# Performance work log

Hardware: AMD Instinct MI355X
Metric: run time of the kernel (lower is better)

Reference implementation:

```python
import jax, jax.numpy as jnp
import numpy as np

N_USERS = 100000
N_ITEMS = 50000
N_NODES = N_USERS + N_ITEMS
LATENT = 64
NNZ = 2400000
BATCH = 2048
EPS = 1e-12  # F.normalize eps


def setup_inputs() -> dict:
    key = jax.random.key(0)
    ks = jax.random.split(key, 16)
    inp = {
        "rows": jax.random.randint(ks[0], (NNZ,), 0, N_NODES, dtype=jnp.int32),
        "cols": jax.random.randint(ks[1], (NNZ,), 0, N_NODES, dtype=jnp.int32),
        "vals": jax.random.uniform(ks[2], (NNZ,), dtype=jnp.float32),
        "x": jax.random.normal(ks[3], (N_NODES, LATENT), dtype=jnp.float32) * 0.1,
        "users": jax.random.randint(ks[12], (BATCH,), 0, N_USERS, dtype=jnp.int32),
        "items": jax.random.randint(ks[13], (BATCH,), 0, N_ITEMS, dtype=jnp.int32),
    }
    for k in range(2):
        inp[f"W_gc{k}"] = jax.random.normal(ks[4 + 4 * k], (LATENT, LATENT), dtype=jnp.float32) * 0.1
        inp[f"b_gc{k}"] = jax.random.normal(ks[5 + 4 * k], (1, LATENT), dtype=jnp.float32) * 0.1
        inp[f"W_bi{k}"] = jax.random.normal(ks[6 + 4 * k], (LATENT, LATENT), dtype=jnp.float32) * 0.1
        inp[f"b_bi{k}"] = jax.random.normal(ks[7 + 4 * k], (1, LATENT), dtype=jnp.float32) * 0.1
    return inp


def _l2_normalize(v):
    # F.normalize(p=2, dim=1): divide by max(||v||_2, eps)
    n = jnp.sqrt(jnp.sum(v * v, axis=1, keepdims=True))
    return v / jnp.maximum(n, EPS)


def reference(rows, cols, vals, x,
              W_gc0, b_gc0, W_bi0, b_bi0,
              W_gc1, b_gc1, W_bi1, b_bi1,
              users, items):
    weights = [(W_gc0, b_gc0, W_bi0, b_bi0), (W_gc1, b_gc1, W_bi1, b_bi1)]
    ego = x                      # [N, D]
    embs = [x]
    for (Wg, bg, Wb, bb) in weights:
        # sparse adj @ ego  (COO gather + segment-sum scatter)
        msgs = vals[:, None] * ego[cols]                              # [nnz, D]
        side = jax.ops.segment_sum(msgs, rows, num_segments=N_NODES)  # [N, D]
        sum_emb = side @ Wg + bg
        bi_emb = (ego * side) @ Wb + bb
        ego = _l2_normalize(jax.nn.leaky_relu(sum_emb + bi_emb, negative_slope=0.2))
        embs.append(ego)
    all_emb = jnp.concatenate(embs, axis=1)          # [N, 3*D]
    users_emb = all_emb[users]                       # [B, 3*D]
    items_emb = all_emb[N_USERS + items]             # [B, 3*D]
    gamma = jnp.sum(users_emb * items_emb, axis=1)   # [B]
    return gamma
```

## Files before the change

### kernel.cpp

```cpp
#include <hip/hip_runtime.h>

#define N_USERS_C 100000
#define N_NODES_C 150000
#define D 64
#define NB 2344
#define NSUP 74
#define CPAD 16
#define TILE1 32
#define SPAD 33
#define SPAD2 17
#define FCAP 1536
#define S1B 256
#define FRAG 240
#define S2CAP 2560
#define BPS 16
#define FPB (S1B / BPS)
#define NSCAN 147
#define MARK 1

__global__ __launch_bounds__(256) void mark1_k(
    const int* __restrict__ u, const int* __restrict__ it,
    unsigned char* __restrict__ samp, unsigned char* __restrict__ need, int batch)
{
    int i = blockIdx.x * blockDim.x + threadIdx.x;
    if (i >= 2 * batch) return;
    int n = (i < batch) ? u[i] : N_USERS_C + it[i - batch];
    samp[n] = MARK;
    need[n] = MARK;
}

__global__ __launch_bounds__(256) void mark2_k(
    const int* __restrict__ rows, const int* __restrict__ cols,
    const unsigned char* __restrict__ samp, unsigned char* __restrict__ need, int nnz)
{
    int gtid = blockIdx.x * blockDim.x + threadIdx.x;
    int stride = gridDim.x * blockDim.x;
    for (int e = gtid; e < nnz; e += stride)
        if (samp[rows[e]] == MARK) need[cols[e]] = MARK;
}

__global__ __launch_bounds__(1024) void scan1_k(
    const unsigned char* __restrict__ need, int* __restrict__ part,
    int* __restrict__ bsum, int n)
{
    __shared__ int wsum[16];
    int i = blockIdx.x * 1024 + threadIdx.x;
    int lane = threadIdx.x & 63, wid = threadIdx.x >> 6;
    int v = (i < n && need[i] == MARK) ? 1 : 0;
    int incl = v;
    #pragma unroll
    for (int off = 1; off < 64; off <<= 1) {
        int t = __shfl_up(incl, off);
        if (lane >= off) incl += t;
    }
    if (lane == 63) wsum[wid] = incl;
    __syncthreads();
    int woff = 0;
    for (int w = 0; w < wid; ++w) woff += wsum[w];
    if (i < n) part[i] = woff + incl - v;
    if (threadIdx.x == 1023) bsum[blockIdx.x] = woff + incl;
}

__global__ __launch_bounds__(256) void scanB_k(
    const int* __restrict__ bsum, int* __restrict__ idx,
    const unsigned char* __restrict__ need, int* __restrict__ list,
    int* __restrict__ bcur, int* __restrict__ Mptr, int n)
{
    __shared__ int pre[NSCAN + 1];
    __shared__ int raw[NSCAN];
    int t = threadIdx.x;
    if (t < NSCAN) raw[t] = bsum[t];
    __syncthreads();
    if (t == 0) {
        int run = 0;
        for (int k = 0; k < NSCAN; ++k) { pre[k] = run; run += raw[k]; }
        pre[NSCAN] = run;
    }
    __syncthreads();
    int i = blockIdx.x * blockDim.x + t;
    if (i < NB) bcur[i * CPAD] = i * FCAP;
    if (blockIdx.x == 0 && t == 0) Mptr[0] = pre[NSCAN];
    if (i >= n) return;
    int val = idx[i] + pre[i >> 10];
    if (need[i] == MARK) { idx[i] = val; list[val] = i; }
    else idx[i] = -1;
}

__global__ __launch_bounds__(512) void s1_k(
    const int* __restrict__ rows, const int* __restrict__ cols,
    const float* __restrict__ vals, const int* __restrict__ idx,
    int2* __restrict__ pairs1, int* __restrict__ scnt, int nnz)
{
    __shared__ int lcur[NSUP];
    int t = threadIdx.x;
    for (int i = t; i < NSUP; i += 512) lcur[i] = 0;
    __syncthreads();
    int b = blockIdx.x;
    int per = (nnz + S1B - 1) / S1B;
    int s = b * per;
    int e = min(nnz, s + per);
    for (int i = s + t; i < e; i += 512) {
        int ci = idx[rows[i]];
        if (ci < 0) continue;
        int sp = ci >> 11;
        int k = atomicAdd(&lcur[sp], 1);
        pairs1[(size_t)sp * (S1B * FRAG) + b * FRAG + k] =
            make_int2(((ci & 2047) << 18) | cols[i], __float_as_int(vals[i]));
    }
    __syncthreads();
    for (int i = t; i < NSUP; i += 512) scnt[i * S1B + b] = lcur[i];
}

__global__ __launch_bounds__(256) void s2_k(
    const int* __restrict__ scnt, const int2* __restrict__ pairs1,
    int* __restrict__ bcurP, int2* __restrict__ pairs)
{
    __shared__ int2 sbuf[S2CAP];
    __shared__ int fcnt[32], fcur[32], gb[32];
    int sp = blockIdx.x / BPS, part = blockIdx.x % BPS;
    int t = threadIdx.x;
    if (t < 32) { fcnt[t] = 0; fcur[t] = 0; }
    __syncthreads();
    int base = 0;
    for (int fi = 0; fi < FPB; ++fi) {
        int b = part * FPB + fi;
        int m = scnt[sp * S1B + b];
        const int2* src = &pairs1[(size_t)sp * (S1B * FRAG) + b * FRAG];
        for (int i = t; i < m; i += 256) {
            int2 p = src[i];
            sbuf[base + i] = p;
            atomicAdd(&fcnt[(p.x >> 18) >> 6], 1);
        }
        base += m;
    }
    __syncthreads();
    if (t < 32) {
        int c = fcnt[t];
        gb[t] = c ? atomicAdd(&bcurP[(sp * 32 + t) * CPAD], c) : 0;
    }
    __syncthreads();
    for (int i = t; i < base; i += 256) {
        int2 p = sbuf[i];
        int ris = p.x >> 18;
        int f = ris >> 6;
        int k = atomicAdd(&fcur[f], 1);
        pairs[gb[f] + k] = make_int2(((ris & 63) << 18) | (p.x & 0x3FFFF), p.y);
    }
}

__global__ __launch_bounds__(256) void sortb_k(
    const int* __restrict__ bcurP, int2* __restrict__ pairs,
    int* __restrict__ rp)
{
    __shared__ int2 buf[FCAP];
    __shared__ int cnt[64];
    __shared__ int cur[64];
    int b = blockIdx.x;
    int s = b * FCAP;
    int e = bcurP[b * CPAD];
    int m = e - s;
    int t = threadIdx.x;
    if (t < 64) cnt[t] = 0;
    __syncthreads();
    for (int i = t; i < m; i += 256) {
        int2 p = pairs[s + i];
        buf[i] = p;
        atomicAdd(&cnt[p.x >> 18], 1);
    }
    __syncthreads();
    if (t < 64) {
        int v = cnt[t];
        int incl = v;
        #pragma unroll
        for (int o = 1; o < 64; o <<= 1) {
            int u = __shfl_up(incl, o);
            if (t >= o) incl += u;
        }
        cur[t] = incl - v;
        rp[b * 65 + t] = s + incl - v;
        if (t == 63) rp[b * 65 + 64] = s + incl;
    }
    __syncthreads();
    for (int i = t; i < m; i += 256) {
        int2 p = buf[i];
        int dst = atomicAdd(&cur[p.x >> 18], 1);
        pairs[s + dst] = make_int2(p.x & 0x3FFFF, p.y);
    }
}

__global__ __launch_bounds__(128, 4) void fuse1_k(
    const int* __restrict__ rp, const int2* __restrict__ pairs,
    const float* __restrict__ x,
    const float* __restrict__ Wg, const float* __restrict__ bg,
    const float* __restrict__ Wb, const float* __restrict__ bb,
    float* __restrict__ out, const int* __restrict__ list,
    const int* __restrict__ Mptr)
{
    __shared__ __align__(16) float sAT[D][SPAD];
    __shared__ __align__(16) float sBT[D][SPAD];

    int nr = Mptr[0];
    int r0 = blockIdx.x * TILE1;
    if (r0 >= nr) return;

    int t    = threadIdx.x;
    int lane = t & 63;
    int wid  = t >> 6;
    int lq   = lane & 15;
    int qb   = lane & 48;

    for (int pass = 0; pass < 4; ++pass) {
        int rr  = wid * 16 + pass * 4 + (lane >> 4);
        int row = r0 + rr;
        int valid = row < nr;
        int s = 0, len = 0, er = 0;
        if (valid) {
            int rb = (row >> 6) * 65 + (row & 63);
            s = rp[rb];
            len = rp[rb + 1] - s;
            er = list[row];
        }
        int ml = len;
        ml = max(ml, __shfl_xor(ml, 16));
        ml = max(ml, __shfl_xor(ml, 32));

        float4 acc = make_float4(0.f, 0.f, 0.f, 0.f);
        for (int base = 0; base < ml; base += 16) {
            int2 p = make_int2(0, 0);
            int o = base + lq;
            if (o < len) p = pairs[s + o];
            int rem = len - base;
            rem = min(max(rem, 0), 16);
            int mr = rem;
            mr = max(mr, __shfl_xor(mr, 16));
            mr = max(mr, __shfl_xor(mr, 32));
            int cnt8 = (mr + 7) & ~7;
            for (int j = 0; j < cnt8; j += 8) {
                int c[8]; float v[8]; float4 f[8];
                #pragma unroll
                for (int q = 0; q < 8; ++q) {
                    c[q] = __shfl(p.x, qb | (j + q));
                    v[q] = __int_as_float(__shfl(p.y, qb | (j + q)));
                }
                #pragma unroll
                for (int q = 0; q < 8; ++q)
                    f[q] = *(const float4*)&x[(size_t)c[q] * D + lq * 4];
                #pragma unroll
                for (int q = 0; q < 8; ++q) {
                    acc.x = fmaf(v[q], f[q].x, acc.x);
                    acc.y = fmaf(v[q], f[q].y, acc.y);
                    acc.z = fmaf(v[q], f[q].z, acc.z);
                    acc.w = fmaf(v[q], f[q].w, acc.w);
                }
            }
        }
        float4 ev = make_float4(0.f, 0.f, 0.f, 0.f);
        if (valid) ev = *(const float4*)&x[(size_t)er * D + lq * 4];
        sAT[lq * 4 + 0][rr] = acc.x;
        sAT[lq * 4 + 1][rr] = acc.y;
        sAT[lq * 4 + 2][rr] = acc.z;
        sAT[lq * 4 + 3][rr] = acc.w;
        sBT[lq * 4 + 0][rr] = acc.x * ev.x;
        sBT[lq * 4 + 1][rr] = acc.y * ev.y;
        sBT[lq * 4 + 2][rr] = acc.z * ev.z;
        sBT[lq * 4 + 3][rr] = acc.w * ev.w;
    }
    __syncthreads();

    int tc = t & 15;
    int tr = t >> 4;
    float acc2[4][4] = {};
    #pragma unroll 4
    for (int k = 0; k < D; ++k) {
        float av[4] = {sAT[k][tr], sAT[k][tr + 8], sAT[k][tr + 16], sAT[k][tr + 24]};
        float bv[4] = {sBT[k][tr], sBT[k][tr + 8], sBT[k][tr + 16], sBT[k][tr + 24]};
        float4 g4 = *(const float4*)&Wg[k * D + tc * 4];
        float4 w4 = *(const float4*)&Wb[k * D + tc * 4];
        float gv[4] = {g4.x, g4.y, g4.z, g4.w};
        float wv[4] = {w4.x, w4.y, w4.z, w4.w};
        #pragma unroll
        for (int i = 0; i < 4; ++i)
            #pragma unroll
            for (int j = 0; j < 4; ++j)
                acc2[i][j] = fmaf(av[i], gv[j], fmaf(bv[i], wv[j], acc2[i][j]));
    }

    float4 bgv = *(const float4*)&bg[tc * 4];
    float4 bbv = *(const float4*)&bb[tc * 4];
    float bias[4] = {bgv.x + bbv.x, bgv.y + bbv.y, bgv.z + bbv.z, bgv.w + bbv.w};

    float vv[4][4];
    float ss[4] = {0.f, 0.f, 0.f, 0.f};
    #pragma unroll
    for (int i = 0; i < 4; ++i) {
        #pragma unroll
        for (int j = 0; j < 4; ++j) {
            float v = acc2[i][j] + bias[j];
            v = (v > 0.0f) ? v : 0.2f * v;
            vv[i][j] = v;
            ss[i] += v * v;
        }
    }
    #pragma unroll
    for (int i = 0; i < 4; ++i) {
        #pragma unroll
        for (int off = 1; off < 16; off <<= 1)
            ss[i] += __shfl_xor(ss[i], off);
    }
    #pragma unroll
    for (int i = 0; i < 4; ++i) {
        int row = r0 + tr + i * 8;
        if (row < nr) {
            int er2 = list[row];
            float inv = 1.0f / fmaxf(sqrtf(ss[i]), 1e-12f);
            float4 o = make_float4(vv[i][0] * inv, vv[i][1] * inv,
                                   vv[i][2] * inv, vv[i][3] * inv);
            *(float4*)&out[(size_t)er2 * D + tc * 4] = o;
        }
    }
}

__global__ __launch_bounds__(256, 4) void fuse2_k(
    const int* __restrict__ rp, const int2* __restrict__ pairs,
    const float* __restrict__ e1, const int* __restrict__ idx,
    const float* __restrict__ Wg, const float* __restrict__ bg,
    const float* __restrict__ Wb, const float* __restrict__ bb,
    float* __restrict__ out, const int* __restrict__ u,
    const int* __restrict__ it, int batch)
{
    __shared__ __align__(16) float sAT[D][SPAD2];
    __shared__ __align__(16) float sBT[D][SPAD2];

    int nr = 2 * batch;
    int r0 = blockIdx.x * 16;
    if (r0 >= nr) return;

    int t    = threadIdx.x;
    int lane = t & 63;
    int wid  = t >> 6;
    int lq   = lane & 15;
    int qb   = lane & 48;

    {
        int rr  = wid * 4 + (lane >> 4);
        int row = r0 + rr;
        int valid = row < nr;
        int s = 0, len = 0, n = 0;
        if (valid) {
            n = (row < batch) ? u[row] : N_USERS_C + it[row - batch];
            int cr = idx[n];
            int rb = (cr >> 6) * 65 + (cr & 63);
            s = rp[rb];
            len = rp[rb + 1] - s;
        }
        int ml = len;
        ml = max(ml, __shfl_xor(ml, 16));
        ml = max(ml, __shfl_xor(ml, 32));

        float4 acc = make_float4(0.f, 0.f, 0.f, 0.f);
        for (int base = 0; base < ml; base += 16) {
            int2 p = make_int2(0, 0);
            int o = base + lq;
            if (o < len) p = pairs[s + o];
            int rem = len - base;
            rem = min(max(rem, 0), 16);
            int mr = rem;
            mr = max(mr, __shfl_xor(mr, 16));
            mr = max(mr, __shfl_xor(mr, 32));
            int cnt8 = (mr + 7) & ~7;
            for (int j = 0; j < cnt8; j += 8) {
                int c[8]; float v[8]; float4 f[8];
                #pragma unroll
                for (int q = 0; q < 8; ++q) {
                    c[q] = __shfl(p.x, qb | (j + q));
                    v[q] = __int_as_float(__shfl(p.y, qb | (j + q)));
                }
                #pragma unroll
                for (int q = 0; q < 8; ++q)
                    f[q] = *(const float4*)&e1[(size_t)c[q] * D + lq * 4];
                #pragma unroll
                for (int q = 0; q < 8; ++q) {
                    acc.x = fmaf(v[q], f[q].x, acc.x);
                    acc.y = fmaf(v[q], f[q].y, acc.y);
                    acc.z = fmaf(v[q], f[q].z, acc.z);
                    acc.w = fmaf(v[q], f[q].w, acc.w);
                }
            }
        }
        float4 ev = make_float4(0.f, 0.f, 0.f, 0.f);
        if (valid) ev = *(const float4*)&e1[(size_t)n * D + lq * 4];
        sAT[lq * 4 + 0][rr] = acc.x;
        sAT[lq * 4 + 1][rr] = acc.y;
        sAT[lq * 4 + 2][rr] = acc.z;
        sAT[lq * 4 + 3][rr] = acc.w;
        sBT[lq * 4 + 0][rr] = acc.x * ev.x;
        sBT[lq * 4 + 1][rr] = acc.y * ev.y;
        sBT[lq * 4 + 2][rr] = acc.z * ev.z;
        sBT[lq * 4 + 3][rr] = acc.w * ev.w;
    }
    __syncthreads();

    int tc = t & 15;
    int tr = t >> 4;
    float acc2[4] = {};
    #pragma unroll 4
    for (int k = 0; k < D; ++k) {
        float a0 = sAT[k][tr];
        float b0 = sBT[k][tr];
        float4 g4 = *(const float4*)&Wg[k * D + tc * 4];
        float4 w4 = *(const float4*)&Wb[k * D + tc * 4];
        float gv[4] = {g4.x, g4.y, g4.z, g4.w};
        float wv[4] = {w4.x, w4.y, w4.z, w4.w};
        #pragma unroll
        for (int j = 0; j < 4; ++j)
            acc2[j] = fmaf(a0, gv[j], fmaf(b0, wv[j], acc2[j]));
    }

    float4 bgv = *(const float4*)&bg[tc * 4];
    float4 bbv = *(const float4*)&bb[tc * 4];
    float bias[4] = {bgv.x + bbv.x, bgv.y + bbv.y, bgv.z + bbv.z, bgv.w + bbv.w};

    float vv[4];
    float ss = 0.f;
    #pragma unroll
    for (int j = 0; j < 4; ++j) {
        float v = acc2[j] + bias[j];
        v = (v > 0.0f) ? v : 0.2f * v;
        vv[j] = v;
        ss += v * v;
    }
    #pragma unroll
    for (int off = 1; off < 16; off <<= 1)
        ss += __shfl_xor(ss, off);

    int row = r0 + tr;
    if (row < nr) {
        float inv = 1.0f / fmaxf(sqrtf(ss), 1e-12f);
        float4 o = make_float4(vv[0] * inv, vv[1] * inv, vv[2] * inv, vv[3] * inv);
        *(float4*)&out[(size_t)row * D + tc * 4] = o;
    }
}

__global__ __launch_bounds__(256) void gamma_k(
    const float* __restrict__ x, const float* __restrict__ e1,
    const float* __restrict__ e2c,
    const int* __restrict__ users, const int* __restrict__ items,
    float* __restrict__ gamma, int batch)
{
    int gtid = blockIdx.x * blockDim.x + threadIdx.x;
    int wave = gtid >> 6;
    int lane = threadIdx.x & 63;
    if (wave >= batch) return;
    size_t uu = (size_t)users[wave];
    size_t tt = (size_t)(N_USERS_C + items[wave]);
    float acc = x[uu * D + lane] * x[tt * D + lane]
              + e1[uu * D + lane] * e1[tt * D + lane]
              + e2c[(size_t)wave * D + lane] * e2c[(size_t)(batch + wave) * D + lane];
    #pragma unroll
    for (int off = 1; off < 64; off <<= 1) acc += __shfl_xor(acc, off);
    if (lane == 0) gamma[wave] = acc;
}

extern "C" void kernel_launch(void* const* d_in, const int* in_sizes, int n_in,
                              void* d_out, int out_size, void* d_ws, size_t ws_size,
                              hipStream_t stream) {
    const int*   rows  = (const int*)d_in[0];
    const int*   cols  = (const int*)d_in[1];
    const float* vals  = (const float*)d_in[2];
    const float* x     = (const float*)d_in[3];
    const int*   users = (const int*)d_in[4];
    const int*   items = (const int*)d_in[5];
    const float* Wg0 = (const float*)d_in[6];
    const float* bg0 = (const float*)d_in[7];
    const float* Wb0 = (const float*)d_in[8];
    const float* bb0 = (const float*)d_in[9];
    const float* Wg1 = (const float*)d_in[10];
    const float* bg1 = (const float*)d_in[11];
    const float* Wb1 = (const float*)d_in[12];
    const float* bb1 = (const float*)d_in[13];

    int nnz   = in_sizes[0];
    int batch = in_sizes[4];
    float* out = (float*)d_out;

    size_t emb = (size_t)N_NODES_C * D;
    float* A      = (float*)d_ws;
    float* Sbuf   = A + emb;
    int*   bcur   = (int*)(Sbuf + emb);
    int*   rp     = bcur + NB * CPAD;
    int*   idx    = rp + NB * 65 + 2;
    int*   list   = idx + N_NODES_C;
    int*   bsum   = list + N_NODES_C;
    int*   Mptr   = bsum + 1024;
    int*   scnt   = Mptr + 4;
    unsigned char* need = (unsigned char*)(scnt + NSUP * S1B);
    unsigned char* samp = need + N_NODES_C;
    int2*  pairs  = (int2*)(((size_t)(samp + N_NODES_C) + 15) & ~(size_t)15);

    int2*  pairs1 = (int2*)Sbuf;
    float* e2c    = Sbuf;

    mark1_k<<<(2 * batch + 255) / 256, 256, 0, stream>>>(users, items, samp, need, batch);
    mark2_k<<<1024, 256, 0, stream>>>(rows, cols, samp, need, nnz);
    scan1_k<<<NSCAN, 1024, 0, stream>>>(need, idx, bsum, N_NODES_C);
    scanB_k<<<(N_NODES_C + 255) / 256, 256, 0, stream>>>(bsum, idx, need, list, bcur, Mptr, N_NODES_C);

    s1_k<<<S1B, 512, 0, stream>>>(rows, cols, vals, idx, pairs1, scnt, nnz);
    s2_k<<<NSUP * BPS, 256, 0, stream>>>(scnt, pairs1, bcur, pairs);
    sortb_k<<<NB, 256, 0, stream>>>(bcur, pairs, rp);

    fuse1_k<<<(N_NODES_C + TILE1 - 1) / TILE1, 128, 0, stream>>>(
        rp, pairs, x, Wg0, bg0, Wb0, bb0, A, list, Mptr);

    fuse2_k<<<(2 * batch + 15) / 16, 256, 0, stream>>>(
        rp, pairs, A, idx, Wg1, bg1, Wb1, bb1, e2c, users, items, batch);

    gamma_k<<<(batch * 64 + 255) / 256, 256, 0, stream>>>(
        x, A, e2c, users, items, out, batch);
}
```

Baseline: 243.6 us.

## Replace three-pass bucket sort with degree-histogram CSR build and atomic scatter

The three-stage bucketed sort (s1/s2/sortb) that grouped edges by compacted row is replaced. Row degrees are now counted with global atomics inside the mark pass, prefix-scanned alongside the need flags, and edges of needed rows are scattered straight into a full-node CSR using per-row atomic cursors. This drops two kernel launches and the intermediate pairs1 staging traffic. In exchange it adds 2.4M global atomics for the degree count, plus scatter atomics, and the writes to pairs become random.

```diff
diff --git a/kernel.cpp b/kernel.cpp
--- a/kernel.cpp
+++ b/kernel.cpp
@@ -3,194 +3,114 @@
 #define N_USERS_C 100000
 #define N_NODES_C 150000
 #define D 64
-#define NB 2344
-#define NSUP 74
-#define CPAD 16
 #define TILE1 32
 #define SPAD 33
 #define SPAD2 17
-#define FCAP 1536
-#define S1B 256
-#define FRAG 240
-#define S2CAP 2560
-#define BPS 16
-#define FPB (S1B / BPS)
 #define NSCAN 147
 #define MARK 1
 
-__global__ __launch_bounds__(256) void mark1_k(
+__global__ __launch_bounds__(256) void mark1z_k(
     const int* __restrict__ u, const int* __restrict__ it,
-    unsigned char* __restrict__ samp, unsigned char* __restrict__ need, int batch)
+    unsigned char* __restrict__ samp, unsigned char* __restrict__ need,
+    int* __restrict__ dega, int batch, int n)
 {
     int i = blockIdx.x * blockDim.x + threadIdx.x;
-    if (i >= 2 * batch) return;
-    int n = (i < batch) ? u[i] : N_USERS_C + it[i - batch];
-    samp[n] = MARK;
-    need[n] = MARK;
-}
-
-__global__ __launch_bounds__(256) void mark2_k(
+    if (i < n) dega[i] = 0;
+    if (i < 2 * batch) {
+        int nd = (i < batch) ? u[i] : N_USERS_C + it[i - batch];
+        samp[nd] = MARK;
+        need[nd] = MARK;
+    }
+}
+
+__global__ __launch_bounds__(256) void mark2h_k(
     const int* __restrict__ rows, const int* __restrict__ cols,
-    const unsigned char* __restrict__ samp, unsigned char* __restrict__ need, int nnz)
+    const unsigned char* __restrict__ samp, unsigned char* __restrict__ need,
+    int* __restrict__ dega, int nnz)
 {
     int gtid = blockIdx.x * blockDim.x + threadIdx.x;
     int stride = gridDim.x * blockDim.x;
-    for (int e = gtid; e < nnz; e += stride)
-        if (samp[rows[e]] == MARK) need[cols[e]] = MARK;
-}
-
-__global__ __launch_bounds__(1024) void scan1_k(
-    const unsigned char* __restrict__ need, int* __restrict__ part,
-    int* __restrict__ bsum, int n)
-{
-    __shared__ int wsum[16];
+    for (int e = gtid; e < nnz; e += stride) {
+        int r = rows[e];
+        atomicAdd(&dega[r], 1);
+        if (samp[r] == MARK) need[cols[e]] = MARK;
+    }
+}
+
+__global__ __launch_bounds__(1024) void scan1x_k(
+    const unsigned char* __restrict__ need, const int* __restrict__ dega,
+    int* __restrict__ part, int* __restrict__ partd,
+    int* __restrict__ bsum, int* __restrict__ bsumd, int n)
+{
+    __shared__ int wsum[16], wsumd[16];
     int i = blockIdx.x * 1024 + threadIdx.x;
     int lane = threadIdx.x & 63, wid = threadIdx.x >> 6;
-    int v = (i < n && need[i] == MARK) ? 1 : 0;
-    int incl = v;
+    int f = (i < n && need[i] == MARK) ? 1 : 0;
+    int d = (i < n) ? dega[i] : 0;
+    int fi = f, di = d;
     #pragma unroll
     for (int off = 1; off < 64; off <<= 1) {
-        int t = __shfl_up(incl, off);
-        if (lane >= off) incl += t;
-    }
-    if (lane == 63) wsum[wid] = incl;
+        int t1 = __shfl_up(fi, off);
+        int t2 = __shfl_up(di, off);
+        if (lane >= off) { fi += t1; di += t2; }
+    }
+    if (lane == 63) { wsum[wid] = fi; wsumd[wid] = di; }
     __syncthreads();
-    int woff = 0;
-    for (int w = 0; w < wid; ++w) woff += wsum[w];
-    if (i < n) part[i] = woff + incl - v;
-    if (threadIdx.x == 1023) bsum[blockIdx.x] = woff + incl;
-}
-
-__global__ __launch_bounds__(256) void scanB_k(
-    const int* __restrict__ bsum, int* __restrict__ idx,
+    int wo = 0, wod = 0;
+    for (int w = 0; w < wid; ++w) { wo += wsum[w]; wod += wsumd[w]; }
+    if (i < n) { part[i] = wo + fi - f; partd[i] = wod + di - d; }
+    if (threadIdx.x == 1023) { bsum[blockIdx.x] = wo + fi; bsumd[blockIdx.x] = wod + di; }
+}
+
+__global__ __launch_bounds__(256) void scanBx_k(
+    const int* __restrict__ bsum, const int* __restrict__ bsumd,
+    const int* __restrict__ part, const int* __restrict__ partd,
     const unsigned char* __restrict__ need, int* __restrict__ list,
-    int* __restrict__ bcur, int* __restrict__ Mptr, int n)
+    int* __restrict__ rps, int* __restrict__ cur,
+    int* __restrict__ Mptr, int n)
 {
     __shared__ int pre[NSCAN + 1];
-    __shared__ int raw[NSCAN];
+    __shared__ int prd[NSCAN + 1];
+    __shared__ int raw[NSCAN], rawd[NSCAN];
     int t = threadIdx.x;
-    if (t < NSCAN) raw[t] = bsum[t];
+    if (t < NSCAN) { raw[t] = bsum[t]; rawd[t] = bsumd[t]; }
     __syncthreads();
     if (t == 0) {
-        int run = 0;
-        for (int k = 0; k < NSCAN; ++k) { pre[k] = run; run += raw[k]; }
-        pre[NSCAN] = run;
+        int rf = 0, rd = 0;
+        for (int k = 0; k < NSCAN; ++k) {
+            pre[k] = rf; rf += raw[k];
+            prd[k] = rd; rd += rawd[k];
+        }
+        pre[NSCAN] = rf; prd[NSCAN] = rd;
     }
     __syncthreads();
     int i = blockIdx.x * blockDim.x + t;
-    if (i < NB) bcur[i * CPAD] = i * FCAP;
     if (blockIdx.x == 0 && t == 0) Mptr[0] = pre[NSCAN];
     if (i >= n) return;
-    int val = idx[i] + pre[i >> 10];
-    if (need[i] == MARK) { idx[i] = val; list[val] = i; }
-    else idx[i] = -1;
-}
-
-__global__ __launch_bounds__(512) void s1_k(
+    int P = partd[i] + prd[i >> 10];
+    rps[i] = P;
+    cur[i] = P;
+    if (need[i] == MARK) list[part[i] + pre[i >> 10]] = i;
+}
+
+__global__ __launch_bounds__(256) void scatter_k(
     const int* __restrict__ rows, const int* __restrict__ cols,
-    const float* __restrict__ vals, const int* __restrict__ idx,
-    int2* __restrict__ pairs1, int* __restrict__ scnt, int nnz)
-{
-    __shared__ int lcur[NSUP];
-    int t = threadIdx.x;
-    for (int i = t; i < NSUP; i += 512) lcur[i] = 0;
-    __syncthreads();
-    int b = blockIdx.x;
-    int per = (nnz + S1B - 1) / S1B;
-    int s = b * per;
-    int e = min(nnz, s + per);
-    for (int i = s + t; i < e; i += 512) {
-        int ci = idx[rows[i]];
-        if (ci < 0) continue;
-        int sp = ci >> 11;
-        int k = atomicAdd(&lcur[sp], 1);
-        pairs1[(size_t)sp * (S1B * FRAG) + b * FRAG + k] =
-            make_int2(((ci & 2047) << 18) | cols[i], __float_as_int(vals[i]));
-    }
-    __syncthreads();
-    for (int i = t; i < NSUP; i += 512) scnt[i * S1B + b] = lcur[i];
-}
-
-__global__ __launch_bounds__(256) void s2_k(
-    const int* __restrict__ scnt, const int2* __restrict__ pairs1,
-    int* __restrict__ bcurP, int2* __restrict__ pairs)
-{
-    __shared__ int2 sbuf[S2CAP];
-    __shared__ int fcnt[32], fcur[32], gb[32];
-    int sp = blockIdx.x / BPS, part = blockIdx.x % BPS;
-    int t = threadIdx.x;
-    if (t < 32) { fcnt[t] = 0; fcur[t] = 0; }
-    __syncthreads();
-    int base = 0;
-    for (int fi = 0; fi < FPB; ++fi) {
-        int b = part * FPB + fi;
-        int m = scnt[sp * S1B + b];
-        const int2* src = &pairs1[(size_t)sp * (S1B * FRAG) + b * FRAG];
-        for (int i = t; i < m; i += 256) {
-            int2 p = src[i];
-            sbuf[base + i] = p;
-            atomicAdd(&fcnt[(p.x >> 18) >> 6], 1);
-        }
-        base += m;
-    }
-    __syncthreads();
-    if (t < 32) {
-        int c = fcnt[t];
-        gb[t] = c ? atomicAdd(&bcurP[(sp * 32 + t) * CPAD], c) : 0;
-    }
-    __syncthreads();
-    for (int i = t; i < base; i += 256) {
-        int2 p = sbuf[i];
-        int ris = p.x >> 18;
-        int f = ris >> 6;
-        int k = atomicAdd(&fcur[f], 1);
-        pairs[gb[f] + k] = make_int2(((ris & 63) << 18) | (p.x & 0x3FFFF), p.y);
-    }
-}
-
-__global__ __launch_bounds__(256) void sortb_k(
-    const int* __restrict__ bcurP, int2* __restrict__ pairs,
-    int* __restrict__ rp)
-{
-    __shared__ int2 buf[FCAP];
-    __shared__ int cnt[64];
-    __shared__ int cur[64];
-    int b = blockIdx.x;
-    int s = b * FCAP;
-    int e = bcurP[b * CPAD];
-    int m = e - s;
-    int t = threadIdx.x;
-    if (t < 64) cnt[t] = 0;
-    __syncthreads();
-    for (int i = t; i < m; i += 256) {
-        int2 p = pairs[s + i];
-        buf[i] = p;
-        atomicAdd(&cnt[p.x >> 18], 1);
-    }
-    __syncthreads();
-    if (t < 64) {
-        int v = cnt[t];
-        int incl = v;
-        #pragma unroll
-        for (int o = 1; o < 64; o <<= 1) {
-            int u = __shfl_up(incl, o);
-            if (t >= o) incl += u;
-        }
-        cur[t] = incl - v;
-        rp[b * 65 + t] = s + incl - v;
-        if (t == 63) rp[b * 65 + 64] = s + incl;
-    }
-    __syncthreads();
-    for (int i = t; i < m; i += 256) {
-        int2 p = buf[i];
-        int dst = atomicAdd(&cur[p.x >> 18], 1);
-        pairs[s + dst] = make_int2(p.x & 0x3FFFF, p.y);
+    const float* __restrict__ vals, const unsigned char* __restrict__ need,
+    int* __restrict__ cur, int2* __restrict__ pairs, int nnz)
+{
+    int gtid = blockIdx.x * blockDim.x + threadIdx.x;
+    int stride = gridDim.x * blockDim.x;
+    for (int e = gtid; e < nnz; e += stride) {
+        int r = rows[e];
+        if (need[r] != MARK) continue;
+        int pos = atomicAdd(&cur[r], 1);
+        pairs[pos] = make_int2(cols[e], __float_as_int(vals[e]));
     }
 }
 
 __global__ __launch_bounds__(128, 4) void fuse1_k(
-    const int* __restrict__ rp, const int2* __restrict__ pairs,
-    const float* __restrict__ x,
+    const int* __restrict__ rps, const int* __restrict__ curp,
+    const int2* __restrict__ pairs, const float* __restrict__ x,
     const float* __restrict__ Wg, const float* __restrict__ bg,
     const float* __restrict__ Wb, const float* __restrict__ bb,
     float* __restrict__ out, const int* __restrict__ list,
@@ -215,10 +135,9 @@
         int valid = row < nr;
         int s = 0, len = 0, er = 0;
         if (valid) {
-            int rb = (row >> 6) * 65 + (row & 63);
-            s = rp[rb];
-            len = rp[rb + 1] - s;
             er = list[row];
+            s = rps[er];
+            len = curp[er] - s;
         }
         int ml = len;
         ml = max(ml, __shfl_xor(ml, 16));
@@ -321,8 +240,8 @@
 }
 
 __global__ __launch_bounds__(256, 4) void fuse2_k(
-    const int* __restrict__ rp, const int2* __restrict__ pairs,
-    const float* __restrict__ e1, const int* __restrict__ idx,
+    const int* __restrict__ rps, const int* __restrict__ curp,
+    const int2* __restrict__ pairs, const float* __restrict__ e1,
     const float* __restrict__ Wg, const float* __restrict__ bg,
     const float* __restrict__ Wb, const float* __restrict__ bb,
     float* __restrict__ out, const int* __restrict__ u,
@@ -348,10 +267,8 @@
         int s = 0, len = 0, n = 0;
         if (valid) {
             n = (row < batch) ? u[row] : N_USERS_C + it[row - batch];
-            int cr = idx[n];
-            int rb = (cr >> 6) * 65 + (cr & 63);
-            s = rp[rb];
-            len = rp[rb + 1] - s;
+            s = rps[n];
+            len = curp[n] - s;
         }
         int ml = len;
         ml = max(ml, __shfl_xor(ml, 16));
@@ -486,34 +403,36 @@
     size_t emb = (size_t)N_NODES_C * D;
     float* A      = (float*)d_ws;
     float* Sbuf   = A + emb;
-    int*   bcur   = (int*)(Sbuf + emb);
-    int*   rp     = bcur + NB * CPAD;
-    int*   idx    = rp + NB * 65 + 2;
-    int*   list   = idx + N_NODES_C;
-    int*   bsum   = list + N_NODES_C;
-    int*   Mptr   = bsum + 1024;
-    int*   scnt   = Mptr + 4;
-    unsigned char* need = (unsigned char*)(scnt + NSUP * S1B);
+    int*   rps    = (int*)(Sbuf + emb);
+    int*   cur    = rps + N_NODES_C;
+    int*   dega   = cur + N_NODES_C;
+    int*   list   = dega + N_NODES_C;
+    int*   part   = list + N_NODES_C;
+    int*   partd  = part + N_NODES_C;
+    int*   bsum   = partd + N_NODES_C;
+    int*   bsumd  = bsum + 1024;
+    int*   Mptr   = bsumd + 1024;
+    unsigned char* need = (unsigned char*)(Mptr + 4);
     unsigned char* samp = need + N_NODES_C;
     int2*  pairs  = (int2*)(((size_t)(samp + N_NODES_C) + 15) & ~(size_t)15);
 
-    int2*  pairs1 = (int2*)Sbuf;
     float* e2c    = Sbuf;
 
-    mark1_k<<<(2 * batch + 255) / 256, 256, 0, stream>>>(users, items, samp, need, batch);
-    mark2_k<<<1024, 256, 0, stream>>>(rows, cols, samp, need, nnz);
-    scan1_k<<<NSCAN, 1024, 0, stream>>>(need, idx, bsum, N_NODES_C);
-    scanB_k<<<(N_NODES_C + 255) / 256, 256, 0, stream>>>(bsum, idx, need, list, bcur, Mptr, N_NODES_C);
-
-    s1_k<<<S1B, 512, 0, stream>>>(rows, cols, vals, idx, pairs1, scnt, nnz);
-    s2_k<<<NSUP * BPS, 256, 0, stream>>>(scnt, pairs1, bcur, pairs);
-    sortb_k<<<NB, 256, 0, stream>>>(bcur, pairs, rp);
+    mark1z_k<<<(N_NODES_C + 255) / 256, 256, 0, stream>>>(
+        users, items, samp, need, dega, batch, N_NODES_C);
+    mark2h_k<<<1024, 256, 0, stream>>>(rows, cols, samp, need, dega, nnz);
+
+    scan1x_k<<<NSCAN, 1024, 0, stream>>>(need, dega, part, partd, bsum, bsumd, N_NODES_C);
+    scanBx_k<<<(N_NODES_C + 255) / 256, 256, 0, stream>>>(
+        bsum, bsumd, part, partd, need, list, rps, cur, Mptr, N_NODES_C);
+
+    scatter_k<<<1024, 256, 0, stream>>>(rows, cols, vals, need, cur, pairs, nnz);
 
     fuse1_k<<<(N_NODES_C + TILE1 - 1) / TILE1, 128, 0, stream>>>(
-        rp, pairs, x, Wg0, bg0, Wb0, bb0, A, list, Mptr);
+        rps, cur, pairs, x, Wg0, bg0, Wb0, bb0, A, list, Mptr);
 
     fuse2_k<<<(2 * batch + 15) / 16, 256, 0, stream>>>(
-        rp, pairs, A, idx, Wg1, bg1, Wb1, bb1, e2c, users, items, batch);
+        rps, cur, pairs, A, Wg1, bg1, Wb1, bb1, e2c, users, items, batch);
 
     gamma_k<<<(batch * 64 + 255) / 256, 256, 0, stream>>>(
         x, A, e2c, users, items, out, batch);
```

Measured after the change: 341.2 us. 40.1% more time.

## Fuse marking and compaction scan kernels into one cooperative grid-synced kernel

Applied to the files above, without the earlier changes.

Replaces four small front-end launches (batch marking, neighbor marking, block scan, prefix fixup) with a single cooperative kernel of 1024 blocks that separates phases with grid.sync. The per-block scan now covers 147 nodes using a shared-memory Hillis-Steele scan, and block 0 scans the block sums. The goal is to remove launch gaps and inter-kernel overhead, at the cost of grid-wide barrier latency and the occupancy limits of a cooperative launch.

```diff
diff --git a/kernel.cpp b/kernel.cpp
--- a/kernel.cpp
+++ b/kernel.cpp
@@ -1,4 +1,7 @@
 #include <hip/hip_runtime.h>
+#include <hip/hip_cooperative_groups.h>
+
+namespace cg = cooperative_groups;
 
 #define N_USERS_C 100000
 #define N_NODES_C 150000
@@ -15,75 +18,87 @@
 #define S2CAP 2560
 #define BPS 16
 #define FPB (S1B / BPS)
-#define NSCAN 147
 #define MARK 1
-
-__global__ __launch_bounds__(256) void mark1_k(
+#define CB 1024
+#define CT 256
+#define CHUNK 147
+
+__global__ __launch_bounds__(CT) void front_k(
     const int* __restrict__ u, const int* __restrict__ it,
-    unsigned char* __restrict__ samp, unsigned char* __restrict__ need, int batch)
-{
-    int i = blockIdx.x * blockDim.x + threadIdx.x;
-    if (i >= 2 * batch) return;
-    int n = (i < batch) ? u[i] : N_USERS_C + it[i - batch];
-    samp[n] = MARK;
-    need[n] = MARK;
-}
-
-__global__ __launch_bounds__(256) void mark2_k(
     const int* __restrict__ rows, const int* __restrict__ cols,
-    const unsigned char* __restrict__ samp, unsigned char* __restrict__ need, int nnz)
-{
-    int gtid = blockIdx.x * blockDim.x + threadIdx.x;
-    int stride = gridDim.x * blockDim.x;
-    for (int e = gtid; e < nnz; e += stride)
+    unsigned char* __restrict__ samp, unsigned char* __restrict__ need,
+    int* __restrict__ idx, int* __restrict__ list,
+    int* __restrict__ bcur, int* __restrict__ Mptr,
+    int* __restrict__ bsum, int* __restrict__ bpre,
+    int batch, int nnz, int n)
+{
+    cg::grid_group grid = cg::this_grid();
+    __shared__ int sc[CHUNK];
+    __shared__ int ts[CT];
+
+    int t   = threadIdx.x;
+    int b   = blockIdx.x;
+    int tid = b * CT + t;
+    const int nth = CB * CT;
+
+    for (int i = tid; i < 2 * batch; i += nth) {
+        int nd = (i < batch) ? u[i] : N_USERS_C + it[i - batch];
+        samp[nd] = MARK;
+        need[nd] = MARK;
+    }
+    for (int i = tid; i < NB; i += nth) bcur[i * CPAD] = i * FCAP;
+    __threadfence();
+    grid.sync();
+
+    for (int e = tid; e < nnz; e += nth)
         if (samp[rows[e]] == MARK) need[cols[e]] = MARK;
-}
-
-__global__ __launch_bounds__(1024) void scan1_k(
-    const unsigned char* __restrict__ need, int* __restrict__ part,
-    int* __restrict__ bsum, int n)
-{
-    __shared__ int wsum[16];
-    int i = blockIdx.x * 1024 + threadIdx.x;
-    int lane = threadIdx.x & 63, wid = threadIdx.x >> 6;
-    int v = (i < n && need[i] == MARK) ? 1 : 0;
-    int incl = v;
-    #pragma unroll
-    for (int off = 1; off < 64; off <<= 1) {
-        int t = __shfl_up(incl, off);
-        if (lane >= off) incl += t;
-    }
-    if (lane == 63) wsum[wid] = incl;
-    __syncthreads();
-    int woff = 0;
-    for (int w = 0; w < wid; ++w) woff += wsum[w];
-    if (i < n) part[i] = woff + incl - v;
-    if (threadIdx.x == 1023) bsum[blockIdx.x] = woff + incl;
-}
-
-__global__ __launch_bounds__(256) void scanB_k(
-    const int* __restrict__ bsum, int* __restrict__ idx,
-    const unsigned char* __restrict__ need, int* __restrict__ list,
-    int* __restrict__ bcur, int* __restrict__ Mptr, int n)
-{
-    __shared__ int pre[NSCAN + 1];
-    __shared__ int raw[NSCAN];
-    int t = threadIdx.x;
-    if (t < NSCAN) raw[t] = bsum[t];
-    __syncthreads();
-    if (t == 0) {
-        int run = 0;
-        for (int k = 0; k < NSCAN; ++k) { pre[k] = run; run += raw[k]; }
-        pre[NSCAN] = run;
-    }
-    __syncthreads();
-    int i = blockIdx.x * blockDim.x + t;
-    if (i < NB) bcur[i * CPAD] = i * FCAP;
-    if (blockIdx.x == 0 && t == 0) Mptr[0] = pre[NSCAN];
-    if (i >= n) return;
-    int val = idx[i] + pre[i >> 10];
-    if (need[i] == MARK) { idx[i] = val; list[val] = i; }
-    else idx[i] = -1;
+    __threadfence();
+    grid.sync();
+
+    int base = b * CHUNK;
+    int i0   = base + t;
+    int f    = 0;
+    if (t < CHUNK && i0 < n && need[i0] == MARK) f = 1;
+    if (t < CHUNK) sc[t] = f;
+    __syncthreads();
+    for (int off = 1; off < CHUNK; off <<= 1) {
+        int add = 0;
+        if (t < CHUNK && t >= off) add = sc[t - off];
+        __syncthreads();
+        if (t < CHUNK) sc[t] += add;
+        __syncthreads();
+    }
+    if (t == 0) bsum[b] = sc[CHUNK - 1];
+    __threadfence();
+    grid.sync();
+
+    if (b == 0) {
+        int v[4];
+        int s = 0;
+        #pragma unroll
+        for (int k = 0; k < 4; ++k) { v[k] = bsum[t * 4 + k]; s += v[k]; }
+        ts[t] = s;
+        __syncthreads();
+        for (int off = 1; off < CT; off <<= 1) {
+            int add = (t >= off) ? ts[t - off] : 0;
+            __syncthreads();
+            ts[t] += add;
+            __syncthreads();
+        }
+        int run = ts[t] - s;
+        #pragma unroll
+        for (int k = 0; k < 4; ++k) { bpre[t * 4 + k] = run; run += v[k]; }
+        if (t == CT - 1) Mptr[0] = ts[CT - 1];
+    }
+    __threadfence();
+    grid.sync();
+
+    int pre = bpre[b];
+    if (t < CHUNK && i0 < n) {
+        int excl = pre + sc[t] - f;
+        if (f) { idx[i0] = excl; list[excl] = i0; }
+        else idx[i0] = -1;
+    }
 }
 
 __global__ __launch_bounds__(512) void s1_k(
@@ -491,7 +506,8 @@
     int*   idx    = rp + NB * 65 + 2;
     int*   list   = idx + N_NODES_C;
     int*   bsum   = list + N_NODES_C;
-    int*   Mptr   = bsum + 1024;
+    int*   bpre   = bsum + 1024;
+    int*   Mptr   = bpre + 1024;
     int*   scnt   = Mptr + 4;
     unsigned char* need = (unsigned char*)(scnt + NSUP * S1B);
     unsigned char* samp = need + N_NODES_C;
@@ -500,10 +516,17 @@
     int2*  pairs1 = (int2*)Sbuf;
     float* e2c    = Sbuf;
 
-    mark1_k<<<(2 * batch + 255) / 256, 256, 0, stream>>>(users, items, samp, need, batch);
-    mark2_k<<<1024, 256, 0, stream>>>(rows, cols, samp, need, nnz);
-    scan1_k<<<NSCAN, 1024, 0, stream>>>(need, idx, bsum, N_NODES_C);
-    scanB_k<<<(N_NODES_C + 255) / 256, 256, 0, stream>>>(bsum, idx, need, list, bcur, Mptr, N_NODES_C);
+    {
+        int n_nodes = N_NODES_C;
+        void* cargs[] = {
+            (void*)&users, (void*)&items, (void*)&rows, (void*)&cols,
+            (void*)&samp, (void*)&need, (void*)&idx, (void*)&list,
+            (void*)&bcur, (void*)&Mptr, (void*)&bsum, (void*)&bpre,
+            (void*)&batch, (void*)&nnz, (void*)&n_nodes
+        };
+        hipLaunchCooperativeKernel((void*)front_k, dim3(CB), dim3(CT),
+                                   cargs, 0, stream);
+    }
 
     s1_k<<<S1B, 512, 0, stream>>>(rows, cols, vals, idx, pairs1, scnt, nnz);
     s2_k<<<NSUP * BPS, 256, 0, stream>>>(scnt, pairs1, bcur, pairs);
```

Result: slower. 902.7 us (+270.6%).
